# Performance work log

Measured on AMD Instinct MI355X. Metric: run time of the kernel, lower is better.

Reference implementation:

```python
import jax, jax.numpy as jnp
import numpy as np

B, N, C, H, WS, SS = 16, 4096, 512, 8, 8, 4
HD = C // H
SCALE = HD ** -0.5
NW = N // WS  # number of mask windows (= 512)
B_ = B * NW   # windows-times-batch after the view(-1, WS, C)


def _make_mask():
    # faithful replication of create_mask(), including the non-standard
    # window_partition (reshape->transpose->reshape) used by the repo
    img = np.zeros(N, dtype=np.float32)
    img[N - WS:N - SS] = 1.0
    img[N - SS:] = 2.0
    # window_partition on (1, N, 1) then .view(-1, WS):
    mw = img.reshape(N // WS, WS).T.reshape(N // WS, WS)  # (NW, WS)
    am = mw[:, None, :] - mw[:, :, None]                   # (NW, WS, WS)
    return jnp.asarray(np.where(am != 0.0, -100.0, 0.0).astype(np.float32))

ATTN_MASK = _make_mask()  # (NW, WS, WS)


def _layernorm(x, w, b, eps=1e-5):
    mu = jnp.mean(x, axis=-1, keepdims=True)
    var = jnp.mean((x - mu) ** 2, axis=-1, keepdims=True)
    return (x - mu) * jax.lax.rsqrt(var + eps) * w + b


def setup_inputs() -> dict:
    key = jax.random.key(0)
    ks = jax.random.split(key, 8)
    s = 0.02
    return {
        'x': jax.random.normal(ks[0], (B, N, C), jnp.float32),
        'norm1_w': jnp.ones((C,), jnp.float32),
        'norm1_b': jnp.zeros((C,), jnp.float32),
        'qkv_w': jax.random.normal(ks[1], (C, 3 * C), jnp.float32) * s,
        'qkv_b': jnp.zeros((3 * C,), jnp.float32),
        'proj_w': jax.random.normal(ks[2], (C, C), jnp.float32) * s,
        'proj_b': jnp.zeros((C,), jnp.float32),
        'norm2_w': jnp.ones((C,), jnp.float32),
        'norm2_b': jnp.zeros((C,), jnp.float32),
        'mlp_w1': jax.random.normal(ks[3], (C, 4 * C), jnp.float32) * s,
        'mlp_b1': jnp.zeros((4 * C,), jnp.float32),
        'mlp_w2': jax.random.normal(ks[4], (4 * C, C), jnp.float32) * s,
        'mlp_b2': jnp.zeros((C,), jnp.float32),
    }


def reference(x, norm1_w, norm1_b, qkv_w, qkv_b, proj_w, proj_b,
              norm2_w, norm2_b, mlp_w1, mlp_b1, mlp_w2, mlp_b2):
    shortcut = x
    h = _layernorm(x, norm1_w, norm1_b)
    h = jnp.roll(h, -SS, axis=1)  # shift_size > 0
    # repo's window_partition: (B,N,C) -> (B, N//WS, WS, C) -> perm -> (B*WS, N//WS, C)
    win = h.reshape(B, N // WS, WS, C).transpose(0, 2, 1, 3)
    # then .view(-1, WS, C): reinterpret flat buffer as (B_, WS, C)
    win = win.reshape(B_, WS, C)
    qkv = (win @ qkv_w + qkv_b).reshape(B_, WS, 3, H, HD).transpose(2, 0, 3, 1, 4)
    q, k, v = qkv[0], qkv[1], qkv[2]              # (B_, H, WS, HD)
    attn = jnp.einsum('bhqd,bhkd->bhqk', q, k) * SCALE
    attn = attn.reshape(B, NW, H, WS, WS) + ATTN_MASK[None, :, None]
    attn = jax.nn.softmax(attn.reshape(B_, H, WS, WS), axis=-1)
    out = jnp.einsum('bhqk,bhkd->bqhd', attn, v).reshape(B_, WS, C)
    out = out @ proj_w + proj_b
    # repo's window_reverse on the (B_, WS, C) buffer
    out = out.reshape(B, N // WS, WS, C).transpose(0, 2, 1, 3).reshape(B, N, C)
    out = jnp.roll(out, SS, axis=1)
    x = shortcut + out
    h2 = _layernorm(x, norm2_w, norm2_b)
    h2 = jax.nn.gelu(h2 @ mlp_w1 + mlp_b1, approximate=False)
    return x + (h2 @ mlp_w2 + mlp_b2)
```

## Files before the change

kernel.cpp:

```cpp
#include <hip/hip_runtime.h>
#include <hip/hip_bf16.h>
#include <cstdint>
#include <cstddef>

typedef __hip_bfloat16 BF16;
typedef __bf16 bf16x8 __attribute__((ext_vector_type(8)));
typedef float floatx4 __attribute__((ext_vector_type(4)));

static constexpr size_t OFF_WQKV  = 0;
static constexpr size_t OFF_WPROJ = OFF_WQKV  + (size_t)1536 * 512 * 2;
static constexpr size_t OFF_W1    = OFF_WPROJ + (size_t)512 * 512 * 2;
static constexpr size_t OFF_W2    = OFF_W1    + (size_t)2048 * 512 * 2;
static constexpr size_t OFF_H     = OFF_W2    + (size_t)512 * 2048 * 2;
static constexpr size_t OFF_QKV   = OFF_H     + (size_t)65536 * 512 * 2;
static constexpr size_t OFF_ATTN  = OFF_QKV   + (size_t)65536 * 1536 * 2;
static constexpr size_t OFF_M     = OFF_QKV;

__global__ __launch_bounds__(256) void wprep_all(
    const float* __restrict__ qkvw, const float* __restrict__ projw,
    const float* __restrict__ w1, const float* __restrict__ w2,
    BF16* __restrict__ o_qkv, BF16* __restrict__ o_proj,
    BF16* __restrict__ o_w1, BF16* __restrict__ o_w2) {
  __shared__ float t[64][65];
  int b = blockIdx.x;
  const float* W; BF16* Wt; int K, N, bx, by;
  if (b < 192)      {          W = qkvw;  Wt = o_qkv;  K = 512;  N = 1536; bx = b % 24; by = b / 24; }
  else if (b < 256) { b -= 192; W = projw; Wt = o_proj; K = 512;  N = 512;  bx = b % 8;  by = b / 8; }
  else if (b < 512) { b -= 256; W = w1;    Wt = o_w1;   K = 512;  N = 2048; bx = b % 32; by = b / 32; }
  else              { b -= 512; W = w2;    Wt = o_w2;   K = 2048; N = 512;  bx = b % 8;  by = b / 8; }
  const int n0 = bx * 64, k0 = by * 64;
  const int tid = threadIdx.x;
#pragma unroll
  for (int it = 0; it < 16; ++it) {
    int idx = it * 256 + tid;
    int r = idx >> 6, c = idx & 63;
    t[r][c] = W[(size_t)(k0 + r) * N + (n0 + c)];
  }
  __syncthreads();
#pragma unroll
  for (int it = 0; it < 16; ++it) {
    int idx = it * 256 + tid;
    int r = idx >> 6, c = idx & 63;
    Wt[(size_t)(n0 + r) * K + (k0 + c)] = __float2bfloat16(t[c][r]);
  }
}

__global__ __launch_bounds__(256) void ln_kernel(
    const float* __restrict__ x, const float* __restrict__ w,
    const float* __restrict__ b, BF16* __restrict__ out) {
  const int lane = threadIdx.x & 63;
  const size_t row = (size_t)blockIdx.x * 4 + (threadIdx.x >> 6);
  const float* xr = x + row * 512 + lane * 8;
  float xv[8], wv[8], bv[8];
  *(float4*)&xv[0] = *(const float4*)xr;
  *(float4*)&xv[4] = *(const float4*)(xr + 4);
  *(float4*)&wv[0] = *(const float4*)(w + lane * 8);
  *(float4*)&wv[4] = *(const float4*)(w + lane * 8 + 4);
  *(float4*)&bv[0] = *(const float4*)(b + lane * 8);
  *(float4*)&bv[4] = *(const float4*)(b + lane * 8 + 4);
  float s = 0.0f, ss = 0.0f;
#pragma unroll
  for (int t = 0; t < 8; ++t) { s += xv[t]; ss += xv[t] * xv[t]; }
#pragma unroll
  for (int o = 32; o > 0; o >>= 1) { s += __shfl_xor(s, o); ss += __shfl_xor(ss, o); }
  const float mu = s * (1.0f / 512.0f);
  const float var = ss * (1.0f / 512.0f) - mu * mu;
  const float rs = rsqrtf(var + 1e-5f);
  BF16 ob[8];
#pragma unroll
  for (int t = 0; t < 8; ++t)
    ob[t] = __float2bfloat16((xv[t] - mu) * rs * wv[t] + bv[t]);
  *(uint4*)(out + row * 512 + lane * 8) = *(const uint4*)ob;
}

__device__ __forceinline__ void gload16(const BF16* g, const char* l) {
  __builtin_amdgcn_global_load_lds(
      (const __attribute__((address_space(1))) void*)g,
      (__attribute__((address_space(3))) void*)l, 16, 0, 0);
}

__device__ __forceinline__ int win_src_row(int r) {
  const int b = r >> 12;
  const int s = (r >> 9) & 7;
  const int mm = (r >> 3) & 63;
  const int j = r & 7;
  const int p = (64 * mm + 8 * j + s + 4) & 4095;
  return (b << 12) + p;
}

__device__ __forceinline__ float fast_gelu(float v) {
  const float t = __expf(v * -1.702f);
  return v * __builtin_amdgcn_rcpf(1.0f + t);
}

__device__ __forceinline__ uint2 pack4bf(float a, float b, float c, float d) {
  union { BF16 h[4]; uint2 u; } u;
  u.h[0] = __float2bfloat16(a); u.h[1] = __float2bfloat16(b);
  u.h[2] = __float2bfloat16(c); u.h[3] = __float2bfloat16(d);
  return u.u;
}

#define GATE4 asm volatile("s_waitcnt vmcnt(4)" ::: "memory")
#define GATE2 asm volatile("s_waitcnt vmcnt(2)" ::: "memory")
#define GATE0 asm volatile("s_waitcnt vmcnt(0)" ::: "memory")
#define BAR() __builtin_amdgcn_s_barrier()
#define WAITL() asm volatile("s_waitcnt lgkmcnt(0)" ::: "memory")

template <int ROWMAP, int EPI, int K>
__global__ __launch_bounds__(512, 2) void gemm256(
    const BF16* __restrict__ A, const BF16* __restrict__ Bt,
    const float* __restrict__ bias, const float* __restrict__ resid,
    float* __restrict__ outf, BF16* __restrict__ outb, int Nout) {
  __shared__ __align__(16) char smem[131072];
  const int tid = threadIdx.x, lane = tid & 63, wv = tid >> 6;
  const int wm = wv >> 2, wn = wv & 3;

  const int gx = gridDim.x;
  const int nwg = gx * gridDim.y;
  const int hwid = blockIdx.y * gx + blockIdx.x;
  const int swz = (hwid & 7) * (nwg >> 3) + (hwid >> 3);
  const int bm = swz / gx, bn = swz - bm * gx;
  const int row0 = bm * 256, col0 = bn * 256;

  const int srow = lane >> 3;
  const int scol = ((lane & 7) ^ srow) * 8;
  const BF16* Pa[2][2];
  const BF16* Pb[2][2];
#pragma unroll
  for (int mh = 0; mh < 2; ++mh)
#pragma unroll
    for (int c = 0; c < 2; ++c) {
      int ra = row0 + mh * 128 + c * 64 + wv * 8 + srow;
      if (ROWMAP == 1) ra = win_src_row(ra);
      Pa[mh][c] = A + (size_t)ra * K + scol;
      const int rb = col0 + mh * 128 + c * 64 + wv * 8 + srow;
      Pb[mh][c] = Bt + (size_t)rb * K + scol;
    }
  const int ldsw = wv * 1024;

  const int r16 = lane & 15;
  const int sx0 = (((lane >> 4) + 0) ^ (r16 & 7)) * 16;
  const int sx1 = (((lane >> 4) + 4) ^ (r16 & 7)) * 16;
  const int raby = (wm * 64 + r16) * 128;
  const int rbby = (wn * 32 + r16) * 128;

  floatx4 acc[2][4][2][2];
#pragma unroll
  for (int mh = 0; mh < 2; ++mh)
#pragma unroll
    for (int m2 = 0; m2 < 4; ++m2)
#pragma unroll
      for (int nh = 0; nh < 2; ++nh)
#pragma unroll
        for (int n2 = 0; n2 < 2; ++n2)
          acc[mh][m2][nh][n2] = floatx4{0.f, 0.f, 0.f, 0.f};

  bf16x8 fa[4][2], fb0[2][2], fb1[2][2];

#define STG_A(half, dd) do {                                              \
    gload16(Pa[half][0], smem + (dd)*65536 + (half)*16384 + ldsw);        \
    gload16(Pa[half][1], smem + (dd)*65536 + (half)*16384 + 8192 + ldsw); \
  } while (0)
#define STG_B(half, dd) do {                                                      \
    gload16(Pb[half][0], smem + (dd)*65536 + 32768 + (half)*16384 + ldsw);        \
    gload16(Pb[half][1], smem + (dd)*65536 + 32768 + (half)*16384 + 8192 + ldsw); \
  } while (0)
#define ADV() do {                                          \
    Pa[0][0] += 64; Pa[0][1] += 64; Pa[1][0] += 64; Pa[1][1] += 64; \
    Pb[0][0] += 64; Pb[0][1] += 64; Pb[1][0] += 64; Pb[1][1] += 64; \
  } while (0)

#define RD_FA(mh, dd)                                                          \
  _Pragma("unroll")                                                            \
  for (int m2 = 0; m2 < 4; ++m2) {                                             \
    fa[m2][0] = *(const bf16x8*)(smem + (dd)*65536 + (mh)*16384 + raby + m2*2048 + sx0); \
    fa[m2][1] = *(const bf16x8*)(smem + (dd)*65536 + (mh)*16384 + raby + m2*2048 + sx1); \
  }
#define RD_FB(dst, nh, dd)                                                     \
  _Pragma("unroll")                                                            \
  for (int n2 = 0; n2 < 2; ++n2) {                                             \
    dst[n2][0] = *(const bf16x8*)(smem + (dd)*65536 + 32768 + (nh)*16384 + rbby + n2*2048 + sx0); \
    dst[n2][1] = *(const bf16x8*)(smem + (dd)*65536 + 32768 + (nh)*16384 + rbby + n2*2048 + sx1); \
  }
#define MF(mh, nh, fbx)                                                        \
  __builtin_amdgcn_s_setprio(1);                                               \
  _Pragma("unroll")                                                            \
  for (int ks = 0; ks < 2; ++ks)                                               \
    _Pragma("unroll")                                                          \
    for (int m2 = 0; m2 < 4; ++m2)                                             \
      _Pragma("unroll")                                                        \
      for (int n2 = 0; n2 < 2; ++n2)                                           \
        acc[mh][m2][nh][n2] = __builtin_amdgcn_mfma_f32_16x16x32_bf16(         \
            fbx[n2][ks], fa[m2][ks], acc[mh][m2][nh][n2], 0, 0, 0);            \
  __builtin_amdgcn_s_setprio(0)

  STG_A(0, 0);
  STG_B(0, 0);
  STG_B(1, 0);
  STG_A(1, 0);
  ADV();
  GATE4;
  BAR();

  constexpr int NT = K / 64;
  for (int t = 0; t < NT - 1; ++t) {
    const int dd = t & 1, de = dd ^ 1;
    RD_FA(0, dd); RD_FB(fb0, 0, dd);
    STG_A(0, de);
    WAITL();
    MF(0, 0, fb0);
    GATE4; BAR();
    RD_FB(fb1, 1, dd);
    STG_B(0, de);
    WAITL();
    MF(0, 1, fb1);
    GATE4; BAR();
    RD_FA(1, dd);
    STG_B(1, de);
    WAITL();
    MF(1, 1, fb1);
    BAR();
    STG_A(1, de);
    MF(1, 0, fb0);
    GATE4; BAR();
    ADV();
  }
  {
    const int dd = (NT - 1) & 1;
    RD_FA(0, dd); RD_FB(fb0, 0, dd);
    WAITL();
    MF(0, 0, fb0);
    GATE2; BAR();
    RD_FB(fb1, 1, dd);
    WAITL();
    MF(0, 1, fb1);
    GATE0; BAR();
    RD_FA(1, dd);
    WAITL();
    MF(1, 1, fb1);
    MF(1, 0, fb0);
  }
#undef STG_A
#undef STG_B
#undef ADV
#undef RD_FA
#undef RD_FB
#undef MF

  const int g4 = (lane >> 4) * 4;
  float4 bsv[2][2];
#pragma unroll
  for (int nh = 0; nh < 2; ++nh)
#pragma unroll
    for (int n2 = 0; n2 < 2; ++n2)
      bsv[nh][n2] = *(const float4*)&bias[col0 + nh * 128 + wn * 32 + n2 * 16 + g4];

#pragma unroll
  for (int mh = 0; mh < 2; ++mh)
#pragma unroll
    for (int m2 = 0; m2 < 4; ++m2) {
      const int r = row0 + mh * 128 + wm * 64 + m2 * 16 + r16;
      size_t rowbase;
      if (EPI == 2) {
        const int b = r >> 12;
        const int np = (r >> 3) & 511;
        const int ap = r & 7;
        const int io = ((ap << 9) + np + 4) & 4095;
        rowbase = ((size_t)(b << 12) + io) * 512;
      } else {
        rowbase = (size_t)r * Nout;
      }
#pragma unroll
      for (int nh = 0; nh < 2; ++nh)
#pragma unroll
        for (int n2 = 0; n2 < 2; ++n2) {
          const int c0 = col0 + nh * 128 + wn * 32 + n2 * 16 + g4;
          floatx4 v = acc[mh][m2][nh][n2];
          v[0] += bsv[nh][n2].x; v[1] += bsv[nh][n2].y;
          v[2] += bsv[nh][n2].z; v[3] += bsv[nh][n2].w;
          if (EPI == 0) {
            *(uint2*)&outb[rowbase + c0] = pack4bf(v[0], v[1], v[2], v[3]);
          } else if (EPI == 1) {
            *(uint2*)&outb[rowbase + c0] = pack4bf(
                fast_gelu(v[0]), fast_gelu(v[1]), fast_gelu(v[2]), fast_gelu(v[3]));
          } else if (EPI == 2) {
            const float4 rv = *(const float4*)&resid[rowbase + c0];
            float4 ov = {rv.x + v[0], rv.y + v[1], rv.z + v[2], rv.w + v[3]};
            *(float4*)&outf[rowbase + c0] = ov;
          } else {
            float4 ov = *(float4*)&outf[rowbase + c0];
            ov.x += v[0]; ov.y += v[1]; ov.z += v[2]; ov.w += v[3];
            *(float4*)&outf[rowbase + c0] = ov;
          }
        }
    }
}

__global__ __launch_bounds__(64) void attn_kernel(
    const BF16* __restrict__ qkv, BF16* __restrict__ out) {
  const int w = blockIdx.x;
  const int lane = threadIdx.x;
  const int qi = lane >> 3, kj = lane & 7;
  __shared__ __align__(16) BF16 sm[8320];
  const BF16* src = qkv + (size_t)w * 8 * 1536;
#pragma unroll
  for (int it = 0; it < 16; ++it) {
    const int idx = it * 64 + lane;
    const int which = idx >> 9;
    const int r = (idx >> 6) & 7;
    const int c = idx & 63;
    *(uint4*)&sm[which * 4160 + r * 520 + c * 8] =
        *(const uint4*)&src[(size_t)r * 1536 + 512 + which * 512 + c * 8];
  }
  __syncthreads();

  const int s = (w >> 6) & 7, mm = w & 63;
  const int pi = 64 * mm + 8 * qi + s;
  const int pj = 64 * mm + 8 * kj + s;
  const int ri = pi >= 4092 ? 2 : (pi >= 4088 ? 1 : 0);
  const int rj = pj >= 4092 ? 2 : (pj >= 4088 ? 1 : 0);
  const float maskv = (ri != rj) ? -100.0f : 0.0f;

  for (int h = 0; h < 8; ++h) {
    const BF16* qp = src + (size_t)qi * 1536 + h * 64;
    const BF16* kp = &sm[kj * 520 + h * 64];
    float acc = 0.0f;
#pragma unroll
    for (int d0 = 0; d0 < 8; ++d0) {
      bf16x8 qv = *(const bf16x8*)(qp + d0 * 8);
      bf16x8 kv = *(const bf16x8*)(kp + d0 * 8);
#pragma unroll
      for (int t = 0; t < 8; ++t) acc += (float)qv[t] * (float)kv[t];
    }
    float sc = acc * 0.125f + maskv;
    float mx = sc;
    mx = fmaxf(mx, __shfl_xor(mx, 1, 8));
    mx = fmaxf(mx, __shfl_xor(mx, 2, 8));
    mx = fmaxf(mx, __shfl_xor(mx, 4, 8));
    float e = __expf(sc - mx);
    float den = e;
    den += __shfl_xor(den, 1, 8);
    den += __shfl_xor(den, 2, 8);
    den += __shfl_xor(den, 4, 8);
    const float P = e / den;

    float o8[8];
#pragma unroll
    for (int t = 0; t < 8; ++t) o8[t] = 0.0f;
#pragma unroll
    for (int j2 = 0; j2 < 8; ++j2) {
      float p2 = __shfl(P, j2, 8);
      bf16x8 vv = *(const bf16x8*)(&sm[4160 + j2 * 520 + h * 64 + kj * 8]);
#pragma unroll
      for (int t = 0; t < 8; ++t) o8[t] += p2 * (float)vv[t];
    }
    BF16 ob[8];
#pragma unroll
    for (int t = 0; t < 8; ++t) ob[t] = __float2bfloat16(o8[t]);
    *(uint4*)(&out[((size_t)w * 8 + qi) * 512 + h * 64 + kj * 8]) = *(const uint4*)ob;
  }
}

extern "C" void kernel_launch(void* const* d_in, const int* in_sizes, int n_in,
                              void* d_out, int out_size, void* d_ws, size_t ws_size,
                              hipStream_t stream) {
  (void)in_sizes; (void)n_in; (void)out_size; (void)ws_size;
  const float* x     = (const float*)d_in[0];
  const float* n1w   = (const float*)d_in[1];
  const float* n1b   = (const float*)d_in[2];
  const float* qkvw  = (const float*)d_in[3];
  const float* qkvb  = (const float*)d_in[4];
  const float* projw = (const float*)d_in[5];
  const float* projb = (const float*)d_in[6];
  const float* n2w   = (const float*)d_in[7];
  const float* n2b   = (const float*)d_in[8];
  const float* w1    = (const float*)d_in[9];
  const float* b1    = (const float*)d_in[10];
  const float* w2    = (const float*)d_in[11];
  const float* b2    = (const float*)d_in[12];
  float* out = (float*)d_out;
  char* ws = (char*)d_ws;

  BF16* wt_qkv  = (BF16*)(ws + OFF_WQKV);
  BF16* wt_proj = (BF16*)(ws + OFF_WPROJ);
  BF16* wt_w1   = (BF16*)(ws + OFF_W1);
  BF16* wt_w2   = (BF16*)(ws + OFF_W2);
  BF16* hbuf    = (BF16*)(ws + OFF_H);
  BF16* qkvbuf  = (BF16*)(ws + OFF_QKV);
  BF16* attnbuf = (BF16*)(ws + OFF_ATTN);
  BF16* mbuf    = (BF16*)(ws + OFF_M);

  wprep_all<<<768, 256, 0, stream>>>(qkvw, projw, w1, w2,
                                     wt_qkv, wt_proj, wt_w1, wt_w2);

  ln_kernel<<<16384, 256, 0, stream>>>(x, n1w, n1b, hbuf);
  gemm256<1, 0, 512><<<dim3(6, 256), 512, 0, stream>>>(hbuf, wt_qkv, qkvb, nullptr, nullptr, qkvbuf, 1536);
  attn_kernel<<<8192, 64, 0, stream>>>(qkvbuf, attnbuf);
  gemm256<0, 2, 512><<<dim3(2, 256), 512, 0, stream>>>(attnbuf, wt_proj, projb, x, out, nullptr, 512);
  ln_kernel<<<16384, 256, 0, stream>>>(out, n2w, n2b, hbuf);
  gemm256<0, 1, 512><<<dim3(8, 256), 512, 0, stream>>>(hbuf, wt_w1, b1, nullptr, nullptr, mbuf, 2048);
  gemm256<0, 3, 2048><<<dim3(2, 256), 512, 0, stream>>>(mbuf, wt_w2, b2, nullptr, out, nullptr, 512);
}
```

Before: 714.0 us.

## Switch GEMM to 32x32x16 MFMA tiles and stage Q in LDS for attention

The GEMM inner loop now uses 32x32x16 bf16 MFMA instructions with 16-float accumulators in place of 16x16x32. This cuts the instruction count and the LDS fragment reads per FLOP, and the fragment indexing and epilogue column mapping are reworked to match. The attention kernel also copies Q, K and V into shared memory with a padded row stride, so Q is no longer read from global memory in every head iteration. The risks are a wrong epilogue layout and higher register pressure under launch_bounds(512,2).

```diff
diff --git a/kernel.cpp b/kernel.cpp
--- a/kernel.cpp
+++ b/kernel.cpp
@@ -6,6 +6,7 @@
 typedef __hip_bfloat16 BF16;
 typedef __bf16 bf16x8 __attribute__((ext_vector_type(8)));
 typedef float floatx4 __attribute__((ext_vector_type(4)));
+typedef float f32x16 __attribute__((ext_vector_type(16)));
 
 static constexpr size_t OFF_WQKV  = 0;
 static constexpr size_t OFF_WPROJ = OFF_WQKV  + (size_t)1536 * 512 * 2;
@@ -100,6 +101,13 @@
   return u.u;
 }
 
+__device__ __forceinline__ f32x16 zero16() {
+  f32x16 z;
+#pragma unroll
+  for (int i = 0; i < 16; ++i) z[i] = 0.0f;
+  return z;
+}
+
 #define GATE4 asm volatile("s_waitcnt vmcnt(4)" ::: "memory")
 #define GATE2 asm volatile("s_waitcnt vmcnt(2)" ::: "memory")
 #define GATE0 asm volatile("s_waitcnt vmcnt(0)" ::: "memory")
@@ -138,24 +146,23 @@
     }
   const int ldsw = wv * 1024;
 
-  const int r16 = lane & 15;
-  const int sx0 = (((lane >> 4) + 0) ^ (r16 & 7)) * 16;
-  const int sx1 = (((lane >> 4) + 4) ^ (r16 & 7)) * 16;
-  const int raby = (wm * 64 + r16) * 128;
-  const int rbby = (wn * 32 + r16) * 128;
-
-  floatx4 acc[2][4][2][2];
+  const int r31 = lane & 31;
+  const int hi = lane >> 5;
+  int sxk[4];
+#pragma unroll
+  for (int ks = 0; ks < 4; ++ks) sxk[ks] = ((ks * 2 + hi) ^ (r31 & 7)) * 16;
+  const int raby = (wm * 64 + r31) * 128;
+  const int rbby = (wn * 32 + r31) * 128;
+
+  f32x16 acc[2][2][2];
 #pragma unroll
   for (int mh = 0; mh < 2; ++mh)
 #pragma unroll
-    for (int m2 = 0; m2 < 4; ++m2)
-#pragma unroll
-      for (int nh = 0; nh < 2; ++nh)
-#pragma unroll
-        for (int n2 = 0; n2 < 2; ++n2)
-          acc[mh][m2][nh][n2] = floatx4{0.f, 0.f, 0.f, 0.f};
-
-  bf16x8 fa[4][2], fb0[2][2], fb1[2][2];
+    for (int m = 0; m < 2; ++m)
+#pragma unroll
+      for (int nh = 0; nh < 2; ++nh) acc[mh][m][nh] = zero16();
+
+  bf16x8 fa[2][4], fb0[4], fb1[4];
 
 #define STG_A(half, dd) do {                                              \
     gload16(Pa[half][0], smem + (dd)*65536 + (half)*16384 + ldsw);        \
@@ -172,26 +179,22 @@
 
 #define RD_FA(mh, dd)                                                          \
   _Pragma("unroll")                                                            \
-  for (int m2 = 0; m2 < 4; ++m2) {                                             \
-    fa[m2][0] = *(const bf16x8*)(smem + (dd)*65536 + (mh)*16384 + raby + m2*2048 + sx0); \
-    fa[m2][1] = *(const bf16x8*)(smem + (dd)*65536 + (mh)*16384 + raby + m2*2048 + sx1); \
-  }
+  for (int m = 0; m < 2; ++m)                                                  \
+    _Pragma("unroll")                                                          \
+    for (int ks = 0; ks < 4; ++ks)                                             \
+      fa[m][ks] = *(const bf16x8*)(smem + (dd)*65536 + (mh)*16384 + raby + m*4096 + sxk[ks]);
 #define RD_FB(dst, nh, dd)                                                     \
   _Pragma("unroll")                                                            \
-  for (int n2 = 0; n2 < 2; ++n2) {                                             \
-    dst[n2][0] = *(const bf16x8*)(smem + (dd)*65536 + 32768 + (nh)*16384 + rbby + n2*2048 + sx0); \
-    dst[n2][1] = *(const bf16x8*)(smem + (dd)*65536 + 32768 + (nh)*16384 + rbby + n2*2048 + sx1); \
-  }
+  for (int ks = 0; ks < 4; ++ks)                                               \
+    dst[ks] = *(const bf16x8*)(smem + (dd)*65536 + 32768 + (nh)*16384 + rbby + sxk[ks]);
 #define MF(mh, nh, fbx)                                                        \
   __builtin_amdgcn_s_setprio(1);                                               \
   _Pragma("unroll")                                                            \
-  for (int ks = 0; ks < 2; ++ks)                                               \
+  for (int ks = 0; ks < 4; ++ks)                                               \
     _Pragma("unroll")                                                          \
-    for (int m2 = 0; m2 < 4; ++m2)                                             \
-      _Pragma("unroll")                                                        \
-      for (int n2 = 0; n2 < 2; ++n2)                                           \
-        acc[mh][m2][nh][n2] = __builtin_amdgcn_mfma_f32_16x16x32_bf16(         \
-            fbx[n2][ks], fa[m2][ks], acc[mh][m2][nh][n2], 0, 0, 0);            \
+    for (int m = 0; m < 2; ++m)                                                \
+      acc[mh][m][nh] = __builtin_amdgcn_mfma_f32_32x32x16_bf16(                \
+          fbx[ks], fa[m][ks], acc[mh][m][nh], 0, 0, 0);                        \
   __builtin_amdgcn_s_setprio(0)
 
   STG_A(0, 0);
@@ -247,19 +250,19 @@
 #undef RD_FB
 #undef MF
 
-  const int g4 = (lane >> 4) * 4;
-  float4 bsv[2][2];
+  const int hi4 = hi * 4;
+  float4 bsv[2][4];
 #pragma unroll
   for (int nh = 0; nh < 2; ++nh)
 #pragma unroll
-    for (int n2 = 0; n2 < 2; ++n2)
-      bsv[nh][n2] = *(const float4*)&bias[col0 + nh * 128 + wn * 32 + n2 * 16 + g4];
+    for (int q = 0; q < 4; ++q)
+      bsv[nh][q] = *(const float4*)&bias[col0 + nh * 128 + wn * 32 + q * 8 + hi4];
 
 #pragma unroll
   for (int mh = 0; mh < 2; ++mh)
 #pragma unroll
-    for (int m2 = 0; m2 < 4; ++m2) {
-      const int r = row0 + mh * 128 + wm * 64 + m2 * 16 + r16;
+    for (int m = 0; m < 2; ++m) {
+      const int r = row0 + mh * 128 + wm * 64 + m * 32 + r31;
       size_t rowbase;
       if (EPI == 2) {
         const int b = r >> 12;
@@ -271,28 +274,31 @@
         rowbase = (size_t)r * Nout;
       }
 #pragma unroll
-      for (int nh = 0; nh < 2; ++nh)
-#pragma unroll
-        for (int n2 = 0; n2 < 2; ++n2) {
-          const int c0 = col0 + nh * 128 + wn * 32 + n2 * 16 + g4;
-          floatx4 v = acc[mh][m2][nh][n2];
-          v[0] += bsv[nh][n2].x; v[1] += bsv[nh][n2].y;
-          v[2] += bsv[nh][n2].z; v[3] += bsv[nh][n2].w;
+      for (int nh = 0; nh < 2; ++nh) {
+        f32x16 a = acc[mh][m][nh];
+#pragma unroll
+        for (int q = 0; q < 4; ++q) {
+          const int c0 = col0 + nh * 128 + wn * 32 + q * 8 + hi4;
+          float v0 = a[q * 4 + 0] + bsv[nh][q].x;
+          float v1 = a[q * 4 + 1] + bsv[nh][q].y;
+          float v2 = a[q * 4 + 2] + bsv[nh][q].z;
+          float v3 = a[q * 4 + 3] + bsv[nh][q].w;
           if (EPI == 0) {
-            *(uint2*)&outb[rowbase + c0] = pack4bf(v[0], v[1], v[2], v[3]);
+            *(uint2*)&outb[rowbase + c0] = pack4bf(v0, v1, v2, v3);
           } else if (EPI == 1) {
             *(uint2*)&outb[rowbase + c0] = pack4bf(
-                fast_gelu(v[0]), fast_gelu(v[1]), fast_gelu(v[2]), fast_gelu(v[3]));
+                fast_gelu(v0), fast_gelu(v1), fast_gelu(v2), fast_gelu(v3));
           } else if (EPI == 2) {
             const float4 rv = *(const float4*)&resid[rowbase + c0];
-            float4 ov = {rv.x + v[0], rv.y + v[1], rv.z + v[2], rv.w + v[3]};
+            float4 ov = {rv.x + v0, rv.y + v1, rv.z + v2, rv.w + v3};
             *(float4*)&outf[rowbase + c0] = ov;
           } else {
             float4 ov = *(float4*)&outf[rowbase + c0];
-            ov.x += v[0]; ov.y += v[1]; ov.z += v[2]; ov.w += v[3];
+            ov.x += v0; ov.y += v1; ov.z += v2; ov.w += v3;
             *(float4*)&outf[rowbase + c0] = ov;
           }
         }
+      }
     }
 }
 
@@ -301,16 +307,14 @@
   const int w = blockIdx.x;
   const int lane = threadIdx.x;
   const int qi = lane >> 3, kj = lane & 7;
-  __shared__ __align__(16) BF16 sm[8320];
+  __shared__ __align__(16) BF16 sm[8 * 1544];
   const BF16* src = qkv + (size_t)w * 8 * 1536;
 #pragma unroll
-  for (int it = 0; it < 16; ++it) {
-    const int idx = it * 64 + lane;
-    const int which = idx >> 9;
-    const int r = (idx >> 6) & 7;
-    const int c = idx & 63;
-    *(uint4*)&sm[which * 4160 + r * 520 + c * 8] =
-        *(const uint4*)&src[(size_t)r * 1536 + 512 + which * 512 + c * 8];
+  for (int rr = 0; rr < 8; ++rr) {
+    const uint4* s4 = (const uint4*)(src + (size_t)rr * 1536);
+    uint4* d4 = (uint4*)(&sm[rr * 1544]);
+#pragma unroll
+    for (int c = 0; c < 3; ++c) d4[c * 64 + lane] = s4[c * 64 + lane];
   }
   __syncthreads();
 
@@ -322,8 +326,8 @@
   const float maskv = (ri != rj) ? -100.0f : 0.0f;
 
   for (int h = 0; h < 8; ++h) {
-    const BF16* qp = src + (size_t)qi * 1536 + h * 64;
-    const BF16* kp = &sm[kj * 520 + h * 64];
+    const BF16* qp = &sm[qi * 1544 + h * 64];
+    const BF16* kp = &sm[kj * 1544 + 512 + h * 64];
     float acc = 0.0f;
 #pragma unroll
     for (int d0 = 0; d0 < 8; ++d0) {
@@ -350,7 +354,7 @@
 #pragma unroll
     for (int j2 = 0; j2 < 8; ++j2) {
       float p2 = __shfl(P, j2, 8);
-      bf16x8 vv = *(const bf16x8*)(&sm[4160 + j2 * 520 + h * 64 + kj * 8]);
+      bf16x8 vv = *(const bf16x8*)(&sm[j2 * 1544 + 1024 + h * 64 + kj * 8]);
 #pragma unroll
       for (int t = 0; t < 8; ++t) o8[t] += p2 * (float)vv[t];
     }
```

Measured after the change: 765.7 us. 7.3% more time.
